# Kernel tuning notes

Measured on AMD Instinct MI355X. Metric: run time of the kernel, lower is better.

The kernel has to match this reference:

```python
import jax, jax.numpy as jnp
import numpy as np

NCLASSES = 21
CONF_THRESH = 0.5
IOU_THRESH = 0.45
TOP_K = 200
NMS_MAX_OUT = 400
NEG = jnp.float32(-1e9)  # sentinel for suppressed / below-threshold scores

B, N_BOXES = 8, 8732
LAST = NCLASSES + 4 * (NCLASSES - 1) + 1  # 102


def setup_inputs() -> dict:
    key = jax.random.key(0)
    kc, kxy, kwh, ke = jax.random.split(key, 4)
    conf = jax.random.uniform(kc, (B, N_BOXES, NCLASSES), dtype=jnp.float32)
    # plausible normalized boxes: xmin,ymin in [0,0.8], width/height in [0.01,0.2]
    xy = jax.random.uniform(kxy, (B, N_BOXES, NCLASSES - 1, 2), minval=0.0, maxval=0.8)
    wh = jax.random.uniform(kwh, (B, N_BOXES, NCLASSES - 1, 2), minval=0.01, maxval=0.2)
    boxes = jnp.concatenate([xy, xy + wh], axis=-1).reshape(B, N_BOXES, 4 * (NCLASSES - 1))
    extra = jax.random.uniform(ke, (B, N_BOXES, 1), dtype=jnp.float32)
    y_pred = jnp.concatenate([conf, boxes, extra], axis=-1)  # [B, N, 102]
    return {"y_pred": y_pred}


def _iou_one_vs_all(box, boxes):
    # box: [4] (xmin,ymin,xmax,ymax); boxes: [N,4]
    x1 = jnp.maximum(box[0], boxes[:, 0])
    y1 = jnp.maximum(box[1], boxes[:, 1])
    x2 = jnp.minimum(box[2], boxes[:, 2])
    y2 = jnp.minimum(box[3], boxes[:, 3])
    inter = jnp.maximum(x2 - x1, 0.0) * jnp.maximum(y2 - y1, 0.0)
    area_a = (box[2] - box[0]) * (box[3] - box[1])
    area_b = (boxes[:, 2] - boxes[:, 0]) * (boxes[:, 3] - boxes[:, 1])
    union = area_a + area_b - inter
    return jnp.where(union > 0.0, inter / union, 0.0)


def _nms_one_class(rows):
    # rows: [N, 7] = (class_id, conf, xmin, ymin, xmax, ymax, extra)
    n = rows.shape[0]
    scores0 = jnp.where(rows[:, 1] > CONF_THRESH, rows[:, 1], NEG)
    boxes = rows[:, 2:6]
    idx_range = jnp.arange(n)

    def step(live, _):
        best = jnp.argmax(live)
        valid = live[best] > NEG * 0.5  # any real score passed the threshold
        ious = _iou_one_vs_all(boxes[best], boxes)
        suppress = valid & ((ious > IOU_THRESH) | (idx_range == best))
        live = jnp.where(suppress, NEG, live)
        return live, (best, valid)

    _, (sel, selv) = jax.lax.scan(step, scores0, None, length=NMS_MAX_OUT)
    # gather selected rows; zero-pad invalid slots (matches tf.pad with 0)
    out = jnp.where(selv[:, None], rows[sel], 0.0)  # [NMS_MAX_OUT, 7]
    return out


def _per_image(item):
    # item: [N, 102]
    n = item.shape[0]
    conf = item[:, 1:NCLASSES]                                  # [N, C-1]
    boxes = item[:, NCLASSES:NCLASSES + 4 * (NCLASSES - 1)].reshape(n, NCLASSES - 1, 4)
    extra = item[:, -1]                                         # [N]
    class_ids = jnp.arange(1, NCLASSES, dtype=item.dtype)       # [C-1]
    rows = jnp.concatenate([
        jnp.broadcast_to(class_ids[:, None, None], (NCLASSES - 1, n, 1)),
        conf.T[:, :, None],
        jnp.transpose(boxes, (1, 0, 2)),
        jnp.broadcast_to(extra[None, :, None], (NCLASSES - 1, n, 1)),
    ], axis=-1)                                                 # [C-1, N, 7]
    per_class = jax.vmap(_nms_one_class)(rows)                  # [C-1, MAX_OUT, 7]
    filtered = per_class.reshape(-1, 7)                         # [(C-1)*MAX_OUT, 7]
    _, top_idx = jax.lax.top_k(filtered[:, 1], TOP_K)           # sorted descending
    return filtered[top_idx]                                    # [TOP_K, 7]


def reference(y_pred):
    return jax.vmap(_per_image)(y_pred)  # [B, TOP_K, 7]
```

## Files before the change

kernel.cpp:

```cpp
#include <hip/hip_runtime.h>
#include <cstdint>

#define NB 8
#define NBOX 8732
#define NCL 21
#define NCM1 20
#define LASTD 102
#define CONF_TH 0.5f
#define IOU_TH 0.45f
#define TOPK 200
#define MAXOUT 400
#define SELCAP 200
#define EMITN 256
#define NTASK (NB * NCM1)
#define THREADS 1024
#define NW 16
#define NIT 9
#define NBIN 2048
#define KPAD 8768
#define NBATCH (KPAD / 64)

#define MIDD ((double)IOU_TH + 0x1p-26)

struct SM {
    float4 selbox[SELCAP];
    float selA[SELCAP];
    uint64_t selkey[SELCAP];
    uint64_t keys[KPAD];
    uint64_t smask[2][64];
    unsigned long long supW[2][NW];
    int hist[NBIN];
    int binstart[NBIN];
    int wavetot[NW];
    int Mshare, nselshare, prevNshare, doneflag;
};

__device__ __forceinline__ int iou_sup(float4 a, float aA, float4 b, float bA) {
    float x1 = fmaxf(a.x, b.x), y1 = fmaxf(a.y, b.y);
    float x2 = fminf(a.z, b.z), y2 = fminf(a.w, b.w);
    float iw = fmaxf(__fsub_rn(x2, x1), 0.0f);
    float ih = fmaxf(__fsub_rn(y2, y1), 0.0f);
    float inter = __fmul_rn(iw, ih);
    float uni = __fsub_rn(__fadd_rn(aA, bA), inter);
    return (double)inter > MIDD * (double)uni;
}

__device__ __forceinline__ float4 load_box(const float* __restrict__ img,
                                           int boxoff, uint64_t key) {
    if ((key >> 32) == 0) return make_float4(0.f, 0.f, 0.f, 0.f);
    uint32_t i = 0xFFFFFFFFu - (uint32_t)key;
    const float* bp = img + (size_t)i * LASTD + boxoff;
    return make_float4(bp[0], bp[1], bp[2], bp[3]);
}

__device__ __forceinline__ float box_area(float4 b) {
    return __fmul_rn(__fsub_rn(b.z, b.x), __fsub_rn(b.w, b.y));
}

__global__ __launch_bounds__(THREADS) void nms_per_class(const float* __restrict__ yp,
                                                         float* __restrict__ rows) {
    __shared__ SM sm;
    const int task = blockIdx.x;
    const int b = task / NCM1;
    const int cm1 = task % NCM1;
    const int tid = threadIdx.x;
    const int lane = tid & 63;
    const int wav = tid >> 6;
    const float* img = yp + (size_t)b * NBOX * LASTD;
    const int boxoff = NCL + 4 * cm1;

    float confs[NIT];
    #pragma unroll
    for (int it = 0; it < NIT; ++it) {
        int idx = it * THREADS + tid;
        confs[it] = (idx < NBOX) ? img[(size_t)idx * LASTD + (1 + cm1)] : 0.0f;
    }
    sm.hist[tid] = 0; sm.hist[tid + THREADS] = 0;
    __syncthreads();

    #pragma unroll
    for (int it = 0; it < NIT; ++it) {
        int idx = it * THREADS + tid;
        if (idx < NBOX && confs[it] > CONF_TH) {
            int bin = (int)((__float_as_uint(confs[it]) - 0x3F000000u) >> 12);
            atomicAdd(&sm.hist[bin], 1);
        }
    }
    __syncthreads();

    int h0 = sm.hist[2 * tid], h1 = sm.hist[2 * tid + 1];
    int x = h0 + h1;
    int s = x;
    #pragma unroll
    for (int d = 1; d <= 32; d <<= 1) {
        int y = __shfl_down(s, d);
        if (lane + d < 64) s += y;
    }
    if (lane == 0) sm.wavetot[wav] = s;
    __syncthreads();
    int cross = 0;
    #pragma unroll
    for (int w = 0; w < NW; ++w)
        if (w > wav) cross += sm.wavetot[w];
    int Safter = cross + s - x;
    sm.binstart[2 * tid + 1] = Safter;
    sm.binstart[2 * tid] = Safter + h1;
    if (tid == 0) sm.Mshare = cross + s;
    sm.hist[2 * tid] = 0; sm.hist[2 * tid + 1] = 0;
    __syncthreads();

    #pragma unroll
    for (int it = 0; it < NIT; ++it) {
        int idx = it * THREADS + tid;
        if (idx < NBOX && confs[it] > CONF_TH) {
            uint32_t bits = __float_as_uint(confs[it]);
            int bin = (int)((bits - 0x3F000000u) >> 12);
            int slot = sm.binstart[bin] + atomicAdd(&sm.hist[bin], 1);
            sm.keys[slot] = ((uint64_t)bits << 32) |
                            (uint32_t)(0xFFFFFFFFu - (uint32_t)idx);
        }
    }
    __syncthreads();
    const int M = sm.Mshare;
    for (int m = M + tid; m < KPAD; m += THREADS) sm.keys[m] = 0;
    for (int f = tid; f < NBIN; f += THREADS) {
        int s0 = sm.binstart[f], h = sm.hist[f];
        for (int i2 = 1; i2 < h; ++i2) {
            uint64_t key = sm.keys[s0 + i2];
            int j = i2 - 1;
            while (j >= 0 && sm.keys[s0 + j] < key) {
                sm.keys[s0 + j + 1] = sm.keys[s0 + j];
                --j;
            }
            sm.keys[s0 + j + 1] = key;
        }
    }
    __syncthreads();

    uint64_t keyC = sm.keys[lane];
    uint64_t keyN = sm.keys[64 + lane];
    float4 boxC = load_box(img, boxoff, keyC);
    float4 boxN = load_box(img, boxoff, keyN);
    float aC = box_area(boxC), aN = box_area(boxN);
    #pragma unroll
    for (int tt = 0; tt < 4; ++tt) {
        int c = wav + tt * NW;
        float4 cb;
        cb.x = __shfl(boxC.x, c); cb.y = __shfl(boxC.y, c);
        cb.z = __shfl(boxC.z, c); cb.w = __shfl(boxC.w, c);
        float ca = __shfl(aC, c);
        uint64_t row = 0;
        if (ca > 0.0f)
            row = __ballot(lane < c && iou_sup(cb, ca, boxC, aC));
        if (lane == 0) sm.smask[0][c] = row;
    }
    if (tid < 2 * NW) ((unsigned long long*)sm.supW)[tid] = 0ull;
    __syncthreads();

    int nsel = 0, prevN = 0;
    bool done = false;
    for (int i = 0; i < NBATCH && !done; ++i) {
        const int p = i & 1;
        const bool vC = (keyC >> 32) != 0;
        {
            int sup = 0;
            for (int j = prevN + wav; j < nsel; j += NW)
                sup |= iou_sup(boxC, aC, sm.selbox[j], sm.selA[j]);
            unsigned long long bal = __ballot(vC && sup);
            if (lane == 0 && bal) atomicOr(&sm.supW[p][wav], bal);
        }
        int f0 = (i + 2) * 64;
        uint64_t key2 = (f0 < KPAD) ? sm.keys[f0 + lane] : 0;
        float4 box2 = load_box(img, boxoff, key2);
        float a2 = box_area(box2);
        __syncthreads();
        const int nselPre = nsel;
        if (wav == 0) {
            unsigned long long V = __ballot(vC);
            unsigned long long E = (lane < NW) ? sm.supW[p][lane] : 0ull;
            #pragma unroll
            for (int d = 1; d < NW; d <<= 1) E |= __shfl_xor(E, d);
            E = __shfl(E, 0);
            if (lane < NW) sm.supW[p][lane] = 0ull;
            uint64_t smc = sm.smask[p][lane];
            uint64_t alive = ~(E | ~V);
            uint64_t accm = 0;
            int cnt = nsel;
            while (alive && cnt < SELCAP) {
                int t = __ffsll((unsigned long long)alive) - 1;
                uint64_t bit = 1ull << t;
                accm |= bit;
                cnt++;
                unsigned long long kill = __ballot((smc >> t) & 1ull);
                alive &= ~(kill | bit);
            }
            if ((accm >> lane) & 1ull) {
                int pos = nsel + __popcll(accm & ((1ull << lane) - 1ull));
                sm.selbox[pos] = boxC;
                sm.selA[pos] = aC;
                sm.selkey[pos] = keyC;
            }
            if (lane == 0) {
                sm.nselshare = cnt;
                sm.prevNshare = nsel;
                sm.doneflag = (cnt >= SELCAP) || (V != ~0ull);
            }
        } else {
            unsigned long long sb = 0;
            for (int c = wav - 1; c < 64; c += NW - 1) {
                float4 cb;
                cb.x = __shfl(boxN.x, c); cb.y = __shfl(boxN.y, c);
                cb.z = __shfl(boxN.z, c); cb.w = __shfl(boxN.w, c);
                float ca = __shfl(aN, c);
                if (!(ca > 0.0f)) {
                    if (lane == 0) sm.smask[p ^ 1][c] = 0;
                    continue;
                }
                bool supc = false;
                for (int j0 = 0; j0 < nselPre && !supc; j0 += 64) {
                    int j = j0 + lane;
                    int hit = (j < nselPre) ?
                        iou_sup(cb, ca, sm.selbox[j], sm.selA[j]) : 0;
                    supc = __ballot(hit) != 0ull;
                }
                uint64_t row = 0;
                if (supc) {
                    sb |= 1ull << c;
                } else {
                    row = __ballot(lane < c && iou_sup(cb, ca, boxN, aN));
                }
                if (lane == 0) sm.smask[p ^ 1][c] = row;
            }
            if (lane == 0) sm.supW[p ^ 1][wav] = sb;
        }
        __syncthreads();
        nsel = sm.nselshare;
        prevN = sm.prevNshare;
        done = sm.doneflag != 0;
        keyC = keyN; boxC = boxN; aC = aN;
        keyN = key2; boxN = box2; aN = a2;
    }

    float* out0 = rows + (size_t)task * MAXOUT * 7;
    for (int r = tid; r < EMITN; r += THREADS) {
        float* o = out0 + (size_t)r * 7;
        if (r < nsel) {
            uint64_t key = sm.selkey[r];
            uint32_t i = 0xFFFFFFFFu - (uint32_t)key;
            float4 bx = sm.selbox[r];
            o[0] = (float)(cm1 + 1);
            o[1] = __uint_as_float((uint32_t)(key >> 32));
            o[2] = bx.x;
            o[3] = bx.y;
            o[4] = bx.z;
            o[5] = bx.w;
            o[6] = img[(size_t)i * LASTD + (LASTD - 1)];
        } else {
            #pragma unroll
            for (int q = 0; q < 7; ++q) o[q] = 0.0f;
        }
    }
}

__global__ __launch_bounds__(THREADS) void topk_per_image(const float* __restrict__ rows,
                                                          float* __restrict__ out) {
    __shared__ uint64_t K[8192];
    const int b = blockIdx.x;
    const int tid = threadIdx.x;
    const float* rb = rows + (size_t)b * (NCM1 * MAXOUT) * 7;

    for (int xx = tid; xx < 8192; xx += THREADS) {
        int list = xx >> 8, r = xx & 255;
        uint64_t k = 0;
        if (list < NCM1) {
            int flat = list * MAXOUT + r;
            float conf = rb[(size_t)flat * 7 + 1];
            k = ((uint64_t)__float_as_uint(conf) << 32) |
                (uint32_t)(0xFFFFFFFFu - (uint32_t)flat);
        }
        K[xx] = k;
    }
    __syncthreads();

    for (int round = 0; round < 5; ++round) {
        int npairs = 16 >> round;
        int sep = 256 << round;
        for (int w = tid; w < npairs * 256; w += THREADS) {
            int p = w >> 8, t = w & 255;
            int A = p * 2 * sep;
            uint64_t a = K[A + t];
            uint64_t c = K[A + sep + 255 - t];
            K[A + t] = a > c ? a : c;
        }
        __syncthreads();
        for (int j = 128; j >= 1; j >>= 1) {
            for (int w = tid; w < npairs * 128; w += THREADS) {
                int p = w >> 7, q = w & 127;
                int t = ((q & ~(j - 1)) << 1) | (q & (j - 1));
                int A = p * 2 * sep;
                uint64_t x0 = K[A + t];
                uint64_t x1 = K[A + t + j];
                if (x0 < x1) { K[A + t] = x1; K[A + t + j] = x0; }
            }
            __syncthreads();
        }
    }

    if (tid < TOPK) {
        uint64_t key = K[tid];
        uint32_t flat = 0xFFFFFFFFu - (uint32_t)key;
        const float* src = rb + (size_t)flat * 7;
        float* o = out + ((size_t)b * TOPK + tid) * 7;
        #pragma unroll
        for (int q = 0; q < 7; ++q) o[q] = src[q];
    }
}

extern "C" void kernel_launch(void* const* d_in, const int* in_sizes, int n_in,
                              void* d_out, int out_size, void* d_ws, size_t ws_size,
                              hipStream_t stream) {
    const float* yp = (const float*)d_in[0];
    float* rows = (float*)d_ws;
    float* out = (float*)d_out;

    hipLaunchKernelGGL(nms_per_class, dim3(NTASK), dim3(THREADS), 0, stream, yp, rows);
    hipLaunchKernelGGL(topk_per_image, dim3(NB), dim3(THREADS), 0, stream, rows, out);
}
```

Baseline: 67.94 us.

## Process NMS candidates in 128-box pairs per barrier round with cross-batch masks

The sequential NMS loop now consumes two 64-candidate batches (A and B) per iteration instead of one, with a cross-suppression mask B-vs-A so wave 0 can resolve both serially. This halves the number of block-wide barrier rounds. The helper waves now precompute masks for the next pair and batch five candidate checks against the selected set together instead of early-exiting per candidate. In exchange each round does more speculative IoU work, and the early-exit ballot is dropped. KPAD is padded to a multiple of 128.

```diff
diff --git a/kernel.cpp b/kernel.cpp
--- a/kernel.cpp
+++ b/kernel.cpp
@@ -17,8 +17,8 @@
 #define NW 16
 #define NIT 9
 #define NBIN 2048
-#define KPAD 8768
-#define NBATCH (KPAD / 64)
+#define KPAD 8832
+#define NPAIR (KPAD / 128)
 
 #define MIDD ((double)IOU_TH + 0x1p-26)
 
@@ -27,8 +27,10 @@
     float selA[SELCAP];
     uint64_t selkey[SELCAP];
     uint64_t keys[KPAD];
-    uint64_t smask[2][64];
-    unsigned long long supW[2][NW];
+    uint64_t smA[2][64];
+    uint64_t smB[2][64];
+    uint64_t smBA[2][64];
+    unsigned long long extA[2], extB[2];
     int hist[NBIN];
     int binstart[NBIN];
     int wavetot[NW];
@@ -55,6 +57,13 @@
 
 __device__ __forceinline__ float box_area(float4 b) {
     return __fmul_rn(__fsub_rn(b.z, b.x), __fsub_rn(b.w, b.y));
+}
+
+__device__ __forceinline__ float4 shfl_box(float4 b, int c) {
+    float4 r;
+    r.x = __shfl(b.x, c); r.y = __shfl(b.y, c);
+    r.z = __shfl(b.z, c); r.w = __shfl(b.w, c);
+    return r;
 }
 
 __global__ __launch_bounds__(THREADS) void nms_per_class(const float* __restrict__ yp,
@@ -137,108 +146,178 @@
     }
     __syncthreads();
 
-    uint64_t keyC = sm.keys[lane];
-    uint64_t keyN = sm.keys[64 + lane];
-    float4 boxC = load_box(img, boxoff, keyC);
-    float4 boxN = load_box(img, boxoff, keyN);
-    float aC = box_area(boxC), aN = box_area(boxN);
+    uint64_t keyA = sm.keys[lane],        keyB = sm.keys[64 + lane];
+    uint64_t keyA2 = sm.keys[128 + lane], keyB2 = sm.keys[192 + lane];
+    float4 boxA = load_box(img, boxoff, keyA);
+    float4 boxB = load_box(img, boxoff, keyB);
+    float4 boxA2 = load_box(img, boxoff, keyA2);
+    float4 boxB2 = load_box(img, boxoff, keyB2);
+    float aA = box_area(boxA), aB = box_area(boxB);
+    float aA2 = box_area(boxA2), aB2 = box_area(boxB2);
     #pragma unroll
     for (int tt = 0; tt < 4; ++tt) {
         int c = wav + tt * NW;
-        float4 cb;
-        cb.x = __shfl(boxC.x, c); cb.y = __shfl(boxC.y, c);
-        cb.z = __shfl(boxC.z, c); cb.w = __shfl(boxC.w, c);
-        float ca = __shfl(aC, c);
-        uint64_t row = 0;
-        if (ca > 0.0f)
-            row = __ballot(lane < c && iou_sup(cb, ca, boxC, aC));
-        if (lane == 0) sm.smask[0][c] = row;
-    }
-    if (tid < 2 * NW) ((unsigned long long*)sm.supW)[tid] = 0ull;
+        float4 cbA = shfl_box(boxA, c);
+        float caA = __shfl(aA, c);
+        uint64_t rA = 0;
+        if (caA > 0.0f)
+            rA = __ballot(lane < c && iou_sup(cbA, caA, boxA, aA));
+        if (lane == 0) sm.smA[0][c] = rA;
+        float4 cbB = shfl_box(boxB, c);
+        float caB = __shfl(aB, c);
+        uint64_t rB = 0, rBA = 0;
+        if (caB > 0.0f) {
+            rB = __ballot(lane < c && iou_sup(cbB, caB, boxB, aB));
+            rBA = __ballot(iou_sup(cbB, caB, boxA, aA));
+        }
+        if (lane == 0) { sm.smB[0][c] = rB; sm.smBA[0][c] = rBA; }
+    }
+    if (tid == 0) {
+        sm.extA[0] = 0; sm.extB[0] = 0; sm.extA[1] = 0; sm.extB[1] = 0;
+    }
     __syncthreads();
 
     int nsel = 0, prevN = 0;
     bool done = false;
-    for (int i = 0; i < NBATCH && !done; ++i) {
-        const int p = i & 1;
-        const bool vC = (keyC >> 32) != 0;
+    for (int m = 0; m < NPAIR && !done; ++m) {
+        const int p = m & 1;
         {
-            int sup = 0;
-            for (int j = prevN + wav; j < nsel; j += NW)
-                sup |= iou_sup(boxC, aC, sm.selbox[j], sm.selA[j]);
-            unsigned long long bal = __ballot(vC && sup);
-            if (lane == 0 && bal) atomicOr(&sm.supW[p][wav], bal);
-        }
-        int f0 = (i + 2) * 64;
-        uint64_t key2 = (f0 < KPAD) ? sm.keys[f0 + lane] : 0;
-        float4 box2 = load_box(img, boxoff, key2);
-        float a2 = box_area(box2);
+            int supA = 0, supB = 0;
+            for (int j = prevN + wav; j < nsel; j += NW) {
+                float4 sbx = sm.selbox[j];
+                float sA = sm.selA[j];
+                supA |= iou_sup(boxA, aA, sbx, sA);
+                supB |= iou_sup(boxB, aB, sbx, sA);
+            }
+            unsigned long long balA = __ballot(supA);
+            unsigned long long balB = __ballot(supB);
+            if (lane == 0) {
+                if (balA) atomicOr(&sm.extA[p], balA);
+                if (balB) atomicOr(&sm.extB[p], balB);
+            }
+        }
+        int f0 = (m + 2) * 128;
+        uint64_t keyA3 = (f0 < KPAD) ? sm.keys[f0 + lane] : 0;
+        uint64_t keyB3 = (f0 < KPAD) ? sm.keys[f0 + 64 + lane] : 0;
+        float4 boxA3 = load_box(img, boxoff, keyA3);
+        float4 boxB3 = load_box(img, boxoff, keyB3);
+        float aA3 = box_area(boxA3), aB3 = box_area(boxB3);
         __syncthreads();
         const int nselPre = nsel;
         if (wav == 0) {
-            unsigned long long V = __ballot(vC);
-            unsigned long long E = (lane < NW) ? sm.supW[p][lane] : 0ull;
-            #pragma unroll
-            for (int d = 1; d < NW; d <<= 1) E |= __shfl_xor(E, d);
-            E = __shfl(E, 0);
-            if (lane < NW) sm.supW[p][lane] = 0ull;
-            uint64_t smc = sm.smask[p][lane];
-            uint64_t alive = ~(E | ~V);
-            uint64_t accm = 0;
+            unsigned long long VA = __ballot((keyA >> 32) != 0);
+            unsigned long long VB = __ballot((keyB >> 32) != 0);
+            unsigned long long EA = sm.extA[p];
+            unsigned long long EB = sm.extB[p];
+            if (lane == 0) { sm.extA[p] = 0ull; sm.extB[p] = 0ull; }
+            uint64_t smcA = sm.smA[p][lane];
+            uint64_t smcB = sm.smB[p][lane];
+            uint64_t rBA  = sm.smBA[p][lane];
+            uint64_t alive = ~(EA | ~VA);
+            uint64_t accmA = 0;
             int cnt = nsel;
             while (alive && cnt < SELCAP) {
                 int t = __ffsll((unsigned long long)alive) - 1;
                 uint64_t bit = 1ull << t;
-                accm |= bit;
+                accmA |= bit;
                 cnt++;
-                unsigned long long kill = __ballot((smc >> t) & 1ull);
+                unsigned long long kill = __ballot((smcA >> t) & 1ull);
                 alive &= ~(kill | bit);
             }
-            if ((accm >> lane) & 1ull) {
-                int pos = nsel + __popcll(accm & ((1ull << lane) - 1ull));
-                sm.selbox[pos] = boxC;
-                sm.selA[pos] = aC;
-                sm.selkey[pos] = keyC;
+            const int cntA = cnt;
+            unsigned long long exB = __ballot((rBA & accmA) != 0ull);
+            alive = ~(EB | ~VB | exB);
+            uint64_t accmB = 0;
+            while (alive && cnt < SELCAP) {
+                int t = __ffsll((unsigned long long)alive) - 1;
+                uint64_t bit = 1ull << t;
+                accmB |= bit;
+                cnt++;
+                unsigned long long kill = __ballot((smcB >> t) & 1ull);
+                alive &= ~(kill | bit);
+            }
+            if ((accmA >> lane) & 1ull) {
+                int pos = nsel + __popcll(accmA & ((1ull << lane) - 1ull));
+                sm.selbox[pos] = boxA; sm.selA[pos] = aA; sm.selkey[pos] = keyA;
+            }
+            if ((accmB >> lane) & 1ull) {
+                int pos = cntA + __popcll(accmB & ((1ull << lane) - 1ull));
+                sm.selbox[pos] = boxB; sm.selA[pos] = aB; sm.selkey[pos] = keyB;
             }
             if (lane == 0) {
                 sm.nselshare = cnt;
                 sm.prevNshare = nsel;
-                sm.doneflag = (cnt >= SELCAP) || (V != ~0ull);
+                sm.doneflag = (cnt >= SELCAP) || (VB != ~0ull);
             }
         } else {
-            unsigned long long sb = 0;
-            for (int c = wav - 1; c < 64; c += NW - 1) {
-                float4 cb;
-                cb.x = __shfl(boxN.x, c); cb.y = __shfl(boxN.y, c);
-                cb.z = __shfl(boxN.z, c); cb.w = __shfl(boxN.w, c);
-                float ca = __shfl(aN, c);
-                if (!(ca > 0.0f)) {
-                    if (lane == 0) sm.smask[p ^ 1][c] = 0;
-                    continue;
+            #pragma unroll
+            for (int pass = 0; pass < 2; ++pass) {
+                float4 bx = pass ? boxB2 : boxA2;
+                float ax = pass ? aB2 : aA2;
+                float4 cb0, cb1, cb2, cb3, cb4;
+                float ca0, ca1, ca2, ca3, ca4;
+                int c0 = wav - 1, c1 = c0 + 15, c2 = c0 + 30, c3 = c0 + 45,
+                    c4 = c0 + 60;
+                cb0 = shfl_box(bx, c0); ca0 = __shfl(ax, c0);
+                cb1 = shfl_box(bx, c1); ca1 = __shfl(ax, c1);
+                cb2 = shfl_box(bx, c2); ca2 = __shfl(ax, c2);
+                cb3 = shfl_box(bx, c3); ca3 = __shfl(ax, c3);
+                cb4 = shfl_box(bx, c4 & 63); ca4 = __shfl(ax, c4 & 63);
+                int t0 = 0, t1 = 0, t2 = 0, t3 = 0, t4 = 0;
+                for (int j0 = 0; j0 < nselPre; j0 += 64) {
+                    int j = j0 + lane;
+                    int jv = j < nselPre;
+                    float4 sbx = sm.selbox[jv ? j : 0];
+                    float sA = sm.selA[jv ? j : 0];
+                    t0 |= jv & iou_sup(cb0, ca0, sbx, sA);
+                    t1 |= jv & iou_sup(cb1, ca1, sbx, sA);
+                    t2 |= jv & iou_sup(cb2, ca2, sbx, sA);
+                    t3 |= jv & iou_sup(cb3, ca3, sbx, sA);
+                    t4 |= jv & iou_sup(cb4, ca4, sbx, sA);
                 }
-                bool supc = false;
-                for (int j0 = 0; j0 < nselPre && !supc; j0 += 64) {
-                    int j = j0 + lane;
-                    int hit = (j < nselPre) ?
-                        iou_sup(cb, ca, sm.selbox[j], sm.selA[j]) : 0;
-                    supc = __ballot(hit) != 0ull;
+                unsigned long long sb = 0;
+                #pragma unroll
+                for (int k = 0; k < 5; ++k) {
+                    int c = c0 + k * 15;
+                    float4 cb = k == 0 ? cb0 : k == 1 ? cb1 : k == 2 ? cb2
+                               : k == 3 ? cb3 : cb4;
+                    float ca = k == 0 ? ca0 : k == 1 ? ca1 : k == 2 ? ca2
+                              : k == 3 ? ca3 : ca4;
+                    int hk = k == 0 ? t0 : k == 1 ? t1 : k == 2 ? t2
+                            : k == 3 ? t3 : t4;
+                    if (c < 64 && ca > 0.0f) {
+                        unsigned long long bal = __ballot(hk);
+                        if (bal) {
+                            sb |= 1ull << c;
+                        } else if (pass == 0) {
+                            uint64_t row = __ballot(lane < c &&
+                                iou_sup(cb, ca, boxA2, aA2));
+                            if (lane == 0) sm.smA[p ^ 1][c] = row;
+                        } else {
+                            uint64_t row = __ballot(lane < c &&
+                                iou_sup(cb, ca, boxB2, aB2));
+                            uint64_t rba = __ballot(iou_sup(cb, ca, boxA2, aA2));
+                            if (lane == 0) {
+                                sm.smB[p ^ 1][c] = row;
+                                sm.smBA[p ^ 1][c] = rba;
+                            }
+                        }
+                    }
                 }
-                uint64_t row = 0;
-                if (supc) {
-                    sb |= 1ull << c;
-                } else {
-                    row = __ballot(lane < c && iou_sup(cb, ca, boxN, aN));
+                if (lane == 0 && sb) {
+                    if (pass == 0) atomicOr(&sm.extA[p ^ 1], sb);
+                    else           atomicOr(&sm.extB[p ^ 1], sb);
                 }
-                if (lane == 0) sm.smask[p ^ 1][c] = row;
-            }
-            if (lane == 0) sm.supW[p ^ 1][wav] = sb;
+            }
         }
         __syncthreads();
         nsel = sm.nselshare;
         prevN = sm.prevNshare;
         done = sm.doneflag != 0;
-        keyC = keyN; boxC = boxN; aC = aN;
-        keyN = key2; boxN = box2; aN = a2;
+        keyA = keyA2; boxA = boxA2; aA = aA2;
+        keyB = keyB2; boxB = boxB2; aB = aB2;
+        keyA2 = keyA3; boxA2 = boxA3; aA2 = aA3;
+        keyB2 = keyB3; boxB2 = boxB3; aB2 = aB3;
     }
 
     float* out0 = rows + (size_t)task * MAXOUT * 7;
```

New measurement: 66.54 us. -2.1%, faster.
